# Performance work log

Hardware: AMD Instinct MI355X
Metric: run time of the kernel (lower is better)

Reference implementation:

```python
import jax, jax.numpy as jnp
import numpy as np

L, NH, H, V, MAXP = 12, 12, 768, 50257, 1024
HD = H // NH
EPS = 1e-5


def setup_inputs() -> dict:
    key = jax.random.key(0)
    ks = iter(jax.random.split(key, 32))
    s = 0.02
    inp = {
        "input_ids": jax.random.randint(next(ks), (8, 1024), 0, V),
        "tok_emb": jax.random.normal(next(ks), (V, H), jnp.float32) * s,
        "pos_emb": jax.random.normal(next(ks), (MAXP, H), jnp.float32) * s,
        "ln1_g": jnp.ones((L, H), jnp.float32),
        "ln1_b": jnp.zeros((L, H), jnp.float32),
        "w_attn": jax.random.normal(next(ks), (L, H, 3 * H), jnp.float32) * s,
        "b_attn": jnp.zeros((L, 3 * H), jnp.float32),
        "w_out": jax.random.normal(next(ks), (L, H, H), jnp.float32) * s,
        "b_out": jnp.zeros((L, H), jnp.float32),
        "ln2_g": jnp.ones((L, H), jnp.float32),
        "ln2_b": jnp.zeros((L, H), jnp.float32),
        "w1": jax.random.normal(next(ks), (L, H, 4 * H), jnp.float32) * s,
        "b1": jnp.zeros((L, 4 * H), jnp.float32),
        "w2": jax.random.normal(next(ks), (L, 4 * H, H), jnp.float32) * s,
        "b2": jnp.zeros((L, H), jnp.float32),
        "lnf_g": jnp.ones((H,), jnp.float32),
        "lnf_b": jnp.zeros((H,), jnp.float32),
    }
    return inp


def _ln(x, g, b):
    mu = jnp.mean(x, axis=-1, keepdims=True)
    var = jnp.var(x, axis=-1, keepdims=True)
    return (x - mu) * jax.lax.rsqrt(var + EPS) * g + b


def _gpt2_forward(input_ids, tok_emb, pos_emb, ln1_g, ln1_b, w_attn, b_attn,
                  w_out, b_out, ln2_g, ln2_b, w1, b1, w2, b2, lnf_g, lnf_b):
    B, S = input_ids.shape
    x = tok_emb[input_ids] + pos_emb[:S]  # [B,S,H]
    # causal mask: True above the diagonal (future positions)
    mask = jnp.triu(jnp.ones((S, S), dtype=bool), k=1)
    inv_sqrt_hd = 1.0 / np.sqrt(HD)
    for l in range(L):
        n1 = _ln(x, ln1_g[l], ln1_b[l])
        qkv = n1 @ w_attn[l] + b_attn[l]  # [B,S,3H]
        q, k, v = jnp.split(qkv, 3, axis=-1)
        q = q.reshape(B, S, NH, HD).transpose(0, 2, 1, 3)
        k = k.reshape(B, S, NH, HD).transpose(0, 2, 1, 3)
        v = v.reshape(B, S, NH, HD).transpose(0, 2, 1, 3)
        scores = jnp.einsum('bhtd,bhsd->bhts', q, k)  # [B,NH,S,S]
        # faithful to source: mask with -10000 BEFORE dividing by sqrt(head_size)
        scores = jnp.where(mask, -10000.0, scores) * inv_sqrt_hd
        probs = jax.nn.softmax(scores, axis=-1)
        attn = jnp.einsum('bhts,bhsd->bhtd', probs, v)
        attn = attn.transpose(0, 2, 1, 3).reshape(B, S, H)
        attn = attn @ w_out[l] + b_out[l]
        x = x + attn
        n2 = _ln(x, ln2_g[l], ln2_b[l])
        h = jax.nn.gelu(n2 @ w1[l] + b1[l], approximate=False)
        x = x + (h @ w2[l] + b2[l])
    x = _ln(x, lnf_g, lnf_b)
    final_encoding = x[:, -1]  # [B,H]
    logits = final_encoding @ tok_emb.T  # tied weights, [B,V]
    return logits, final_encoding


def reference(input_ids, tok_emb, pos_emb, ln1_g, ln1_b, w_attn, b_attn,
              w_out, b_out, ln2_g, ln2_b, w1, b1, w2, b2, lnf_g, lnf_b):
    return _gpt2_forward(input_ids, tok_emb, pos_emb, ln1_g, ln1_b, w_attn,
                         b_attn, w_out, b_out, ln2_g, ln2_b, w1, b1, w2, b2,
                         lnf_g, lnf_b)
```

## Files before the change

### kernel.cpp

```cpp
#include <hip/hip_runtime.h>
#include <cmath>

typedef unsigned short u16;
typedef __bf16 bf16;
typedef __attribute__((ext_vector_type(8))) bf16 bf16x8;
typedef __attribute__((ext_vector_type(4))) float f32x4;

#define DINL __device__ __forceinline__

#define BB 8
#define SS 1024
#define HH 768
#define LL 12
#define NHH 12
#define HDD 64
#define MM 8192
#define VV 50257

DINL u16 f2bf(float f) {
    unsigned int u = __builtin_bit_cast(unsigned int, f);
    u += 0x7fff + ((u >> 16) & 1);
    return (u16)(u >> 16);
}

DINL bf16x8 ld_bf8(const u16* p) { return *(const bf16x8*)p; }

typedef __attribute__((address_space(1))) unsigned int as1_u32;
typedef __attribute__((address_space(3))) unsigned int as3_u32;

DINL void gllds16(const void* g, void* l) {
    __builtin_amdgcn_global_load_lds((as1_u32*)g, (as3_u32*)l, 16, 0, 0);
}

#define BARRIER()                                   \
    do {                                            \
        asm volatile("" ::: "memory");              \
        __builtin_amdgcn_s_barrier();               \
        asm volatile("" ::: "memory");              \
    } while (0)

DINL void xcd_remap(int gx, int& mTile, int& nTile) {
    int i = blockIdx.y * gx + blockIdx.x;
    int xcd = i & 7, j = i >> 3;
    nTile = j % gx;
    mTile = (j / gx) * 8 + xcd;
}

__global__ __launch_bounds__(256) void k_embed(const int* __restrict__ ids,
                                               const float* __restrict__ tok,
                                               const float* __restrict__ pos,
                                               float* __restrict__ x) {
    int tk = blockIdx.x;
    int s = tk & (SS - 1);
    int id = ids[tk];
    const float* tr = tok + (size_t)id * HH;
    const float* pr = pos + (size_t)s * HH;
    float* xr = x + (size_t)tk * HH;
#pragma unroll
    for (int j = 0; j < 3; j++) {
        int d = threadIdx.x + j * 256;
        xr[d] = tr[d] + pr[d];
    }
}

__global__ __launch_bounds__(256) void k_tcvt(const float* __restrict__ src, u16* __restrict__ dst,
                                              int R, int C, size_t sstr, size_t dstr) {
    src += (size_t)blockIdx.z * sstr;
    dst += (size_t)blockIdx.z * dstr;
    __shared__ float t[32][33];
    int tx = threadIdx.x & 31, ty = threadIdx.x >> 5;
    int c0 = blockIdx.x * 32, r0 = blockIdx.y * 32;
#pragma unroll
    for (int p = 0; p < 4; p++)
        t[ty + p * 8][tx] = src[(size_t)(r0 + ty + p * 8) * C + c0 + tx];
    __syncthreads();
#pragma unroll
    for (int p = 0; p < 4; p++)
        dst[(size_t)(c0 + ty + p * 8) * R + r0 + tx] = f2bf(t[tx][ty + p * 8]);
}

template <bool F32OUT>
__global__ __launch_bounds__(256) void k_ln(const float* __restrict__ x, const float* __restrict__ g,
                                            const float* __restrict__ b, void* __restrict__ outp,
                                            int nrows, int rs, int ro) {
    int w = threadIdx.x >> 6, lane = threadIdx.x & 63;
    int row = blockIdx.x * 4 + w;
    if (row >= nrows) return;
    const float4* xr = (const float4*)(x + ((size_t)row * rs + ro) * HH);
    float4 v[3];
    float s = 0.f, s2 = 0.f;
#pragma unroll
    for (int j = 0; j < 3; j++) {
        v[j] = xr[lane + 64 * j];
        s += v[j].x + v[j].y + v[j].z + v[j].w;
        s2 += v[j].x * v[j].x + v[j].y * v[j].y + v[j].z * v[j].z + v[j].w * v[j].w;
    }
#pragma unroll
    for (int off = 32; off; off >>= 1) {
        s += __shfl_xor(s, off, 64);
        s2 += __shfl_xor(s2, off, 64);
    }
    float mu = s * (1.0f / HH);
    float rstd = rsqrtf(s2 * (1.0f / HH) - mu * mu + 1e-5f);
#pragma unroll
    for (int j = 0; j < 3; j++) {
        int d4 = lane + 64 * j;
        float4 gv = ((const float4*)g)[d4];
        float4 bv = ((const float4*)b)[d4];
        float o0 = (v[j].x - mu) * rstd * gv.x + bv.x;
        float o1 = (v[j].y - mu) * rstd * gv.y + bv.y;
        float o2 = (v[j].z - mu) * rstd * gv.z + bv.z;
        float o3 = (v[j].w - mu) * rstd * gv.w + bv.w;
        if (F32OUT) {
            ((float4*)outp)[(size_t)row * (HH / 4) + d4] = make_float4(o0, o1, o2, o3);
        } else {
            ushort4 pk;
            pk.x = f2bf(o0); pk.y = f2bf(o1); pk.z = f2bf(o2); pk.w = f2bf(o3);
            *(ushort4*)((u16*)outp + (size_t)row * HH + d4 * 4) = pk;
        }
    }
}

template <int EPI>
__global__ __launch_bounds__(256) void k_gemm(const u16* __restrict__ A, const u16* __restrict__ BT,
                                              const float* __restrict__ bias,
                                              u16* __restrict__ obuf, u16* __restrict__ qb,
                                              u16* __restrict__ kb, u16* __restrict__ vb,
                                              int N, int K) {
    __shared__ u16 As[3][128 * 32];
    __shared__ u16 Bs[3][128 * 32];
    const int t = threadIdx.x, w = t >> 6, lane = t & 63;
    const int l15 = lane & 15, l4 = lane >> 4;
    const int wr = w >> 1, wc = w & 1;
    int mT, nT;
    xcd_remap(gridDim.x, mT, nT);
    const int m0 = mT * 128, n0 = nT * 128;
    const int KT = K >> 5;

    f32x4 acc[4][4] = {};

    auto stage = [&](int buf, int kt) {
#pragma unroll
        for (int i = 0; i < 2; i++) {
            int idx = w * 2 + i;
            int row = idx * 16 + (lane >> 2);
            int kc = kt * 32 + (((lane & 3) ^ ((lane >> 3) & 3)) * 8);
            gllds16(A + (size_t)(m0 + row) * K + kc, &As[buf][idx * 512]);
            gllds16(BT + (size_t)(n0 + row) * K + kc, &Bs[buf][idx * 512]);
        }
    };

    stage(0, 0);
    if (KT > 1) stage(1, 1);
    const int sw = (l15 >> 1) & 3;

    for (int kt = 0; kt < KT; ++kt) {
        int nb = kt + 2;
        if (nb < KT) {
            stage(nb % 3, nb);
            asm volatile("s_waitcnt vmcnt(8)" ::: "memory");
        } else if (kt + 1 < KT) {
            asm volatile("s_waitcnt vmcnt(4)" ::: "memory");
        } else {
            asm volatile("s_waitcnt vmcnt(0)" ::: "memory");
        }
        BARRIER();

        const u16* ap = As[kt % 3];
        const u16* bp = Bs[kt % 3];
        bf16x8 af[4], bfr[4];
#pragma unroll
        for (int i = 0; i < 4; i++) af[i] = ld_bf8(ap + (wr * 64 + i * 16 + l15) * 32 + ((l4 ^ sw) * 8));
#pragma unroll
        for (int j = 0; j < 4; j++) bfr[j] = ld_bf8(bp + (wc * 64 + j * 16 + l15) * 32 + ((l4 ^ sw) * 8));
        __builtin_amdgcn_s_setprio(1);
#pragma unroll
        for (int i = 0; i < 4; i++)
#pragma unroll
            for (int j = 0; j < 4; j++)
                acc[i][j] = __builtin_amdgcn_mfma_f32_16x16x32_bf16(af[i], bfr[j], acc[i][j], 0, 0, 0);
        __builtin_amdgcn_s_setprio(0);
        BARRIER();
    }

#pragma unroll
    for (int i = 0; i < 4; i++) {
#pragma unroll
        for (int j = 0; j < 4; j++) {
#pragma unroll
            for (int r = 0; r < 4; r++) {
                int row = m0 + wr * 64 + i * 16 + l4 * 4 + r;
                int n = n0 + wc * 64 + j * 16 + l15;
                float v = acc[i][j][r] + bias[n];
                if (EPI == 0) {
                    int sg = n / HH, wi = n % HH;
                    int h = wi >> 6, d = wi & 63;
                    int bi = row >> 10, s = row & (SS - 1);
                    size_t bh = (size_t)(bi * NHH + h);
                    if (sg == 0)
                        qb[(bh * SS + s) * HDD + d] = f2bf(v * 0.125f);
                    else if (sg == 1)
                        kb[(bh * SS + s) * HDD + d] = f2bf(v);
                    else
                        vb[(bh * HDD + d) * SS + s] = f2bf(v);
                } else {
                    float gl = 0.5f * v * (1.0f + erff(v * 0.70710678118654752f));
                    obuf[(size_t)row * N + n] = f2bf(gl);
                }
            }
        }
    }
}

__global__ __launch_bounds__(256) void k_gemm64(const u16* __restrict__ A, const u16* __restrict__ BT,
                                                const float* __restrict__ bias, float* __restrict__ xio,
                                                int N, int K) {
    __shared__ u16 As[3][128 * 32];
    __shared__ u16 Bs[3][64 * 32];
    const int t = threadIdx.x, w = t >> 6, lane = t & 63;
    const int l15 = lane & 15, l4 = lane >> 4;
    const int wr = w >> 1, wc = w & 1;
    int mT, nT;
    xcd_remap(gridDim.x, mT, nT);
    const int m0 = mT * 128, n0 = nT * 64;
    const int KT = K >> 5;

    f32x4 acc[4][2] = {};

    auto stage = [&](int buf, int kt) {
        int rr = lane >> 2;
        int kc = kt * 32 + (((lane & 3) ^ ((lane >> 3) & 3)) * 8);
#pragma unroll
        for (int i = 0; i < 2; i++) {
            int idx = w * 2 + i;
            gllds16(A + (size_t)(m0 + idx * 16 + rr) * K + kc, &As[buf][idx * 512]);
        }
        gllds16(BT + (size_t)(n0 + w * 16 + rr) * K + kc, &Bs[buf][w * 512]);
    };

    stage(0, 0);
    if (KT > 1) stage(1, 1);
    const int sw = (l15 >> 1) & 3;

    for (int kt = 0; kt < KT; ++kt) {
        int nb = kt + 2;
        if (nb < KT) {
            stage(nb % 3, nb);
            asm volatile("s_waitcnt vmcnt(6)" ::: "memory");
        } else if (kt + 1 < KT) {
            asm volatile("s_waitcnt vmcnt(3)" ::: "memory");
        } else {
            asm volatile("s_waitcnt vmcnt(0)" ::: "memory");
        }
        BARRIER();

        const u16* ap = As[kt % 3];
        const u16* bp = Bs[kt % 3];
        bf16x8 af[4], bfr[2];
#pragma unroll
        for (int i = 0; i < 4; i++) af[i] = ld_bf8(ap + (wr * 64 + i * 16 + l15) * 32 + ((l4 ^ sw) * 8));
#pragma unroll
        for (int j = 0; j < 2; j++) bfr[j] = ld_bf8(bp + (wc * 32 + j * 16 + l15) * 32 + ((l4 ^ sw) * 8));
        __builtin_amdgcn_s_setprio(1);
#pragma unroll
        for (int i = 0; i < 4; i++)
#pragma unroll
            for (int j = 0; j < 2; j++)
                acc[i][j] = __builtin_amdgcn_mfma_f32_16x16x32_bf16(af[i], bfr[j], acc[i][j], 0, 0, 0);
        __builtin_amdgcn_s_setprio(0);
        BARRIER();
    }

#pragma unroll
    for (int i = 0; i < 4; i++) {
#pragma unroll
        for (int j = 0; j < 2; j++) {
#pragma unroll
            for (int r = 0; r < 4; r++) {
                int row = m0 + wr * 64 + i * 16 + l4 * 4 + r;
                int n = n0 + wc * 32 + j * 16 + l15;
                xio[(size_t)row * N + n] += acc[i][j][r] + bias[n];
            }
        }
    }
}

__global__ __launch_bounds__(256) void k_attn(const u16* __restrict__ q, const u16* __restrict__ k,
                                              const u16* __restrict__ vt, u16* __restrict__ o) {
    int qt = 15 - blockIdx.x;
    int bh = blockIdx.y;
    int w = threadIdx.x >> 6, lane = threadIdx.x & 63;
    int l15 = lane & 15, l4 = lane >> 4;

    __shared__ u16 Ks[2][64 * 64];
    __shared__ u16 Vs[2][64 * 64];
    __shared__ u16 pl[4][16 * 72];
    u16* pw = pl[w];

    const size_t bhq = (size_t)bh * SS * HDD;
    int qrow0 = qt * 64 + w * 16;

    auto stage = [&](int buf, int kvb) {
#pragma unroll
        for (int i = 0; i < 2; i++) {
            int rl = w * 16 + i * 8 + (lane >> 3);
            int c = lane & 7;
            int sc = (c ^ (rl & 7)) * 8;
            gllds16(k + bhq + (size_t)(kvb * 64 + rl) * HDD + sc, &Ks[buf][(w * 16 + i * 8) * 64]);
            gllds16(vt + ((size_t)bh * HDD + rl) * SS + kvb * 64 + sc, &Vs[buf][(w * 16 + i * 8) * 64]);
        }
    };

    bf16x8 aq[2];
#pragma unroll
    for (int ks = 0; ks < 2; ks++)
        aq[ks] = ld_bf8(q + bhq + (size_t)(qrow0 + l15) * HDD + ks * 32 + l4 * 8);

    f32x4 acc[4] = {};
    float mrun[4], psum[4];
#pragma unroll
    for (int r = 0; r < 4; r++) { mrun[r] = -1e30f; psum[r] = 0.f; }

    stage(0, 0);
    __syncthreads();
    int buf = 0;

    for (int kvb = 0; kvb <= qt; ++kvb) {
        if (kvb < qt) stage(buf ^ 1, kvb + 1);

        f32x4 s[4] = {};
#pragma unroll
        for (int c = 0; c < 4; c++) {
#pragma unroll
            for (int ks = 0; ks < 2; ks++) {
                bf16x8 kf = ld_bf8(&Ks[buf][(c * 16 + l15) * 64 + ((ks * 4 + l4) ^ (l15 & 7)) * 8]);
                s[c] = __builtin_amdgcn_mfma_f32_16x16x32_bf16(aq[ks], kf, s[c], 0, 0, 0);
            }
        }
        if (kvb == qt) {
#pragma unroll
            for (int c = 0; c < 4; c++) {
                int kvi = kvb * 64 + c * 16 + l15;
#pragma unroll
                for (int r = 0; r < 4; r++) {
                    int qi = qrow0 + l4 * 4 + r;
                    if (kvi > qi) s[c][r] = -1250.0f;
                }
            }
        }
        float lmax[4];
        int ok = 1;
#pragma unroll
        for (int r = 0; r < 4; r++) {
            lmax[r] = fmaxf(fmaxf(s[0][r], s[1][r]), fmaxf(s[2][r], s[3][r]));
            ok &= (lmax[r] <= mrun[r] + 8.f) ? 1 : 0;
        }
        if (!__all(ok)) {
#pragma unroll
            for (int off = 1; off < 16; off <<= 1)
#pragma unroll
                for (int r = 0; r < 4; r++) lmax[r] = fmaxf(lmax[r], __shfl_xor(lmax[r], off, 64));
#pragma unroll
            for (int r = 0; r < 4; r++) {
                float mnew = fmaxf(mrun[r], lmax[r]);
                float ef = __expf(mrun[r] - mnew);
                mrun[r] = mnew;
                psum[r] *= ef;
#pragma unroll
                for (int cd = 0; cd < 4; cd++) acc[cd][r] *= ef;
            }
        }
#pragma unroll
        for (int c = 0; c < 4; c++)
#pragma unroll
            for (int r = 0; r < 4; r++) {
                float pv = __expf(s[c][r] - mrun[r]);
                psum[r] += pv;
                pw[(l4 * 4 + r) * 72 + c * 16 + l15] = f2bf(pv);
            }
#pragma unroll
        for (int ks = 0; ks < 2; ks++) {
            bf16x8 pa = ld_bf8(pw + l15 * 72 + ks * 32 + l4 * 8);
#pragma unroll
            for (int cd = 0; cd < 4; cd++) {
                bf16x8 vf = ld_bf8(&Vs[buf][(cd * 16 + l15) * 64 + ((ks * 4 + l4) ^ (l15 & 7)) * 8]);
                acc[cd] = __builtin_amdgcn_mfma_f32_16x16x32_bf16(pa, vf, acc[cd], 0, 0, 0);
            }
        }
        __syncthreads();
        buf ^= 1;
    }

#pragma unroll
    for (int off = 1; off < 16; off <<= 1)
#pragma unroll
        for (int r = 0; r < 4; r++) psum[r] += __shfl_xor(psum[r], off, 64);

    int b = bh / NHH, h = bh % NHH;
#pragma unroll
    for (int cd = 0; cd < 4; cd++) {
#pragma unroll
        for (int r = 0; r < 4; r++) {
            int qi = qrow0 + l4 * 4 + r;
            float ov = acc[cd][r] / psum[r];
            o[((size_t)b * SS + qi) * HH + h * HDD + cd * 16 + l15] = f2bf(ov);
        }
    }
}

__global__ __launch_bounds__(256) void k_logits(const float* __restrict__ enc,
                                                const float* __restrict__ tok,
                                                float* __restrict__ out) {
    int w = threadIdx.x >> 6, lane = threadIdx.x & 63;
    int v = blockIdx.x * 4 + w;
    if (v >= VV) return;
    const float4* tr = (const float4*)(tok + (size_t)v * HH);
    float a[8];
#pragma unroll
    for (int b = 0; b < 8; b++) a[b] = 0.f;
#pragma unroll
    for (int j = 0; j < 3; j++) {
        float4 t4 = tr[lane + 64 * j];
#pragma unroll
        for (int b = 0; b < 8; b++) {
            float4 e4 = *(const float4*)(enc + (size_t)b * HH + (lane + 64 * j) * 4);
            a[b] += t4.x * e4.x + t4.y * e4.y + t4.z * e4.z + t4.w * e4.w;
        }
    }
#pragma unroll
    for (int off = 32; off; off >>= 1)
#pragma unroll
        for (int b = 0; b < 8; b++) a[b] += __shfl_xor(a[b], off, 64);
    if (lane == 0) {
#pragma unroll
        for (int b = 0; b < 8; b++) out[(size_t)b * VV + v] = a[b];
    }
}

extern "C" void kernel_launch(void* const* d_in, const int* in_sizes, int n_in,
                              void* d_out, int out_size, void* d_ws, size_t ws_size,
                              hipStream_t stream) {
    const int* ids = (const int*)d_in[0];
    const float* tok = (const float*)d_in[1];
    const float* pos = (const float*)d_in[2];
    const float* ln1g = (const float*)d_in[3];
    const float* ln1b = (const float*)d_in[4];
    const float* wat = (const float*)d_in[5];
    const float* bat = (const float*)d_in[6];
    const float* wou = (const float*)d_in[7];
    const float* bou = (const float*)d_in[8];
    const float* ln2g = (const float*)d_in[9];
    const float* ln2b = (const float*)d_in[10];
    const float* w1 = (const float*)d_in[11];
    const float* b1 = (const float*)d_in[12];
    const float* w2 = (const float*)d_in[13];
    const float* b2 = (const float*)d_in[14];
    const float* lnfg = (const float*)d_in[15];
    const float* lnfb = (const float*)d_in[16];

    char* ws = (char*)d_ws;
    float* xw = (float*)(ws + 0);
    u16* nb = (u16*)(ws + 25165824);
    u16* qb = (u16*)(ws + 37748736);
    u16* kb = (u16*)(ws + 50331648);
    u16* vb = (u16*)(ws + 62914560);
    u16* ab = (u16*)(ws + 75497472);
    u16* hb = (u16*)(ws + 88080384);
    u16* wt = (u16*)(ws + 138412032);
    const size_t LSTR = 7077888;
    const size_t WAO = 0, WOO = 1769472, W1O = 2359296, W2O = 4718592;

    float* outf = (float*)d_out;
    float* enc = outf + (size_t)BB * VV;

    k_embed<<<MM, 256, 0, stream>>>(ids, tok, pos, xw);
    k_tcvt<<<dim3(72, 24, 12), 256, 0, stream>>>(wat, wt + WAO, 768, 2304, (size_t)768 * 2304, LSTR);
    k_tcvt<<<dim3(24, 24, 12), 256, 0, stream>>>(wou, wt + WOO, 768, 768, (size_t)768 * 768, LSTR);
    k_tcvt<<<dim3(96, 24, 12), 256, 0, stream>>>(w1, wt + W1O, 768, 3072, (size_t)768 * 3072, LSTR);
    k_tcvt<<<dim3(24, 96, 12), 256, 0, stream>>>(w2, wt + W2O, 3072, 768, (size_t)3072 * 768, LSTR);

    for (int l = 0; l < LL; l++) {
        const u16* wl = wt + (size_t)l * LSTR;
        k_ln<false><<<MM / 4, 256, 0, stream>>>(xw, ln1g + l * HH, ln1b + l * HH, nb, MM, 1, 0);
        k_gemm<0><<<dim3(18, 64), 256, 0, stream>>>(nb, wl + WAO, bat + (size_t)l * 2304,
                                                    nullptr, qb, kb, vb, 2304, 768);
        k_attn<<<dim3(16, 96), 256, 0, stream>>>(qb, kb, vb, ab);
        k_gemm64<<<dim3(12, 64), 256, 0, stream>>>(ab, wl + WOO, bou + (size_t)l * HH, xw, 768, 768);
        k_ln<false><<<MM / 4, 256, 0, stream>>>(xw, ln2g + l * HH, ln2b + l * HH, nb, MM, 1, 0);
        k_gemm<2><<<dim3(24, 64), 256, 0, stream>>>(nb, wl + W1O, b1 + (size_t)l * 3072,
                                                    hb, nullptr, nullptr, nullptr, 3072, 768);
        k_gemm64<<<dim3(12, 64), 256, 0, stream>>>(hb, wl + W2O, b2 + (size_t)l * HH, xw, 768, 3072);
    }
    k_ln<true><<<2, 256, 0, stream>>>(xw, lnfg, lnfb, enc, BB, SS, SS - 1);
    k_logits<<<(VV + 3) / 4, 256, 0, stream>>>(enc, tok, outf);
}
```

Measured before the change: 3.962 ms.

## Restructure GEMM prefetch to drop the trailing barrier and use exp2 softmax

In both GEMM kernels the prefetch of tile kt+2 now happens after the current tile's fragments are read from LDS, which lets the trailing barrier in each k-iteration be removed. The triple buffer keeps the overwritten slot safe. Attention folds log2(e) into the Q scale, the mask value and the rescale threshold, so softmax can use the native exp2 instruction instead of __expf. This cuts one barrier per k-step and the multiply hidden inside exp, at the cost of relying on subtle buffer-reuse ordering.

```diff
diff --git a/kernel.cpp b/kernel.cpp
--- a/kernel.cpp
+++ b/kernel.cpp
@@ -151,19 +151,12 @@
     };
 
     stage(0, 0);
-    if (KT > 1) stage(1, 1);
+    stage(1, 1);
     const int sw = (l15 >> 1) & 3;
 
     for (int kt = 0; kt < KT; ++kt) {
-        int nb = kt + 2;
-        if (nb < KT) {
-            stage(nb % 3, nb);
-            asm volatile("s_waitcnt vmcnt(8)" ::: "memory");
-        } else if (kt + 1 < KT) {
-            asm volatile("s_waitcnt vmcnt(4)" ::: "memory");
-        } else {
-            asm volatile("s_waitcnt vmcnt(0)" ::: "memory");
-        }
+        if (kt + 1 < KT) asm volatile("s_waitcnt vmcnt(4)" ::: "memory");
+        else             asm volatile("s_waitcnt vmcnt(0)" ::: "memory");
         BARRIER();
 
         const u16* ap = As[kt % 3];
@@ -173,6 +166,9 @@
         for (int i = 0; i < 4; i++) af[i] = ld_bf8(ap + (wr * 64 + i * 16 + l15) * 32 + ((l4 ^ sw) * 8));
 #pragma unroll
         for (int j = 0; j < 4; j++) bfr[j] = ld_bf8(bp + (wc * 64 + j * 16 + l15) * 32 + ((l4 ^ sw) * 8));
+
+        if (kt + 2 < KT) stage((kt + 2) % 3, kt + 2);
+
         __builtin_amdgcn_s_setprio(1);
 #pragma unroll
         for (int i = 0; i < 4; i++)
@@ -180,7 +176,6 @@
             for (int j = 0; j < 4; j++)
                 acc[i][j] = __builtin_amdgcn_mfma_f32_16x16x32_bf16(af[i], bfr[j], acc[i][j], 0, 0, 0);
         __builtin_amdgcn_s_setprio(0);
-        BARRIER();
     }
 
 #pragma unroll
@@ -198,7 +193,7 @@
                     int bi = row >> 10, s = row & (SS - 1);
                     size_t bh = (size_t)(bi * NHH + h);
                     if (sg == 0)
-                        qb[(bh * SS + s) * HDD + d] = f2bf(v * 0.125f);
+                        qb[(bh * SS + s) * HDD + d] = f2bf(v * 0.1803368801111204f);
                     else if (sg == 1)
                         kb[(bh * SS + s) * HDD + d] = f2bf(v);
                     else
@@ -239,19 +234,12 @@
     };
 
     stage(0, 0);
-    if (KT > 1) stage(1, 1);
+    stage(1, 1);
     const int sw = (l15 >> 1) & 3;
 
     for (int kt = 0; kt < KT; ++kt) {
-        int nb = kt + 2;
-        if (nb < KT) {
-            stage(nb % 3, nb);
-            asm volatile("s_waitcnt vmcnt(6)" ::: "memory");
-        } else if (kt + 1 < KT) {
-            asm volatile("s_waitcnt vmcnt(3)" ::: "memory");
-        } else {
-            asm volatile("s_waitcnt vmcnt(0)" ::: "memory");
-        }
+        if (kt + 1 < KT) asm volatile("s_waitcnt vmcnt(3)" ::: "memory");
+        else             asm volatile("s_waitcnt vmcnt(0)" ::: "memory");
         BARRIER();
 
         const u16* ap = As[kt % 3];
@@ -261,6 +249,9 @@
         for (int i = 0; i < 4; i++) af[i] = ld_bf8(ap + (wr * 64 + i * 16 + l15) * 32 + ((l4 ^ sw) * 8));
 #pragma unroll
         for (int j = 0; j < 2; j++) bfr[j] = ld_bf8(bp + (wc * 32 + j * 16 + l15) * 32 + ((l4 ^ sw) * 8));
+
+        if (kt + 2 < KT) stage((kt + 2) % 3, kt + 2);
+
         __builtin_amdgcn_s_setprio(1);
 #pragma unroll
         for (int i = 0; i < 4; i++)
@@ -268,7 +259,6 @@
             for (int j = 0; j < 2; j++)
                 acc[i][j] = __builtin_amdgcn_mfma_f32_16x16x32_bf16(af[i], bfr[j], acc[i][j], 0, 0, 0);
         __builtin_amdgcn_s_setprio(0);
-        BARRIER();
     }
 
 #pragma unroll
@@ -344,7 +334,7 @@
 #pragma unroll
                 for (int r = 0; r < 4; r++) {
                     int qi = qrow0 + l4 * 4 + r;
-                    if (kvi > qi) s[c][r] = -1250.0f;
+                    if (kvi > qi) s[c][r] = -1803.3688f;
                 }
             }
         }
@@ -353,7 +343,7 @@
 #pragma unroll
         for (int r = 0; r < 4; r++) {
             lmax[r] = fmaxf(fmaxf(s[0][r], s[1][r]), fmaxf(s[2][r], s[3][r]));
-            ok &= (lmax[r] <= mrun[r] + 8.f) ? 1 : 0;
+            ok &= (lmax[r] <= mrun[r] + 11.5416f) ? 1 : 0;
         }
         if (!__all(ok)) {
 #pragma unroll
@@ -363,7 +353,7 @@
 #pragma unroll
             for (int r = 0; r < 4; r++) {
                 float mnew = fmaxf(mrun[r], lmax[r]);
-                float ef = __expf(mrun[r] - mnew);
+                float ef = __builtin_amdgcn_exp2f(mrun[r] - mnew);
                 mrun[r] = mnew;
                 psum[r] *= ef;
 #pragma unroll
@@ -374,7 +364,7 @@
         for (int c = 0; c < 4; c++)
 #pragma unroll
             for (int r = 0; r < 4; r++) {
-                float pv = __expf(s[c][r] - mrun[r]);
+                float pv = __builtin_amdgcn_exp2f(s[c][r] - mrun[r]);
                 psum[r] += pv;
                 pw[(l4 * 4 + r) * 72 + c * 16 + l15] = f2bf(pv);
             }
```

Result: faster. 3.848 ms (-2.9%).
